# Kernel tuning notes

Hardware: AMD Instinct MI355X
Metric: run time of the kernel (lower is better)

## Reference

```python
import jax, jax.numpy as jnp
import numpy as np

GRID_DIM = 7  # margin = 0, so each grid cell is a disjoint (H//g, W//g) tile


def setup_inputs() -> dict:
    key = jax.random.key(0)
    k1, k2 = jax.random.split(key)
    B, H, W, C = 8, 224, 224, 256
    NQ = 64
    images = jax.random.normal(k1, (B, H, W, C), dtype=jnp.float32)
    queries = jax.random.normal(k2, (NQ, C), dtype=jnp.float32)
    return {"images": images, "queries": queries}


def reference(images, queries):
    # images: [B, H, W, C]; queries: [NQ, C]
    B, H, W, C = images.shape
    g = GRID_DIM
    hs, ws = H // g, W // g  # tile size per grid cell (margin = 0)
    # Crop all g*g cells at once: [B, g, hs, g, ws, C] -> [B, g*g, L, C]
    # Cell index n = i*g + j (i over height, j over width) matches the
    # original positions ordering (pos[0] -> height, pos[1] -> width).
    regions = images.reshape(B, g, hs, g, ws, C)
    regions = regions.transpose(0, 1, 3, 2, 4, 5).reshape(B, g * g, hs * ws, C)
    # keras.layers.Attention default: unscaled dot-product + softmax.
    scores = jnp.einsum('qc,bnlc->bnql', queries, regions)  # [B, g*g, NQ, L]
    attn = jax.nn.softmax(scores, axis=-1)
    out = jnp.einsum('bnql,bnlc->bnqc', attn, regions)      # [B, g*g, NQ, C]
    return out
```

## Files before the change

kernel.cpp:

```cpp
#include <hip/hip_runtime.h>

typedef _Float16 half8 __attribute__((ext_vector_type(8)));
typedef _Float16 half4 __attribute__((ext_vector_type(4)));
typedef __fp16   fp16x2 __attribute__((ext_vector_type(2)));
typedef float f32x4  __attribute__((ext_vector_type(4)));

#define DEVI __device__ __forceinline__

constexpr int Bc = 8;
constexpr int Hc = 224;
constexpr int Wc = 224;
constexpr int Cc = 256;
constexpr int NQ = 64;
constexpr int TS = 32;
constexpr int Lc = TS * TS;
constexpr int KL = 64;
constexpr int NT = Lc / KL;

constexpr long PSTRIDE = 64 * 256 * 2 + 64 * 4 + 64 * 4;
constexpr long WS_NEED = 784 * PSTRIDE;

DEVI int subidx(int l, int c) {
  return ((((l >> 2) << 4) | (c >> 4)) << 6) | (((l & 3) << 4) | (c & 15));
}

DEVI uint ldsoff(const void* p) {
  return (uint)(uintptr_t)(const __attribute__((address_space(3))) char*)p;
}

union PKU { fp16x2 h; uint u; };
DEVI uint pkrtz(float a, float b) { PKU x; x.h = __builtin_amdgcn_cvt_pkrtz(a, b); return x.u; }
union HBU { _Float16 h; ushort u; };
DEVI ushort hbits(float x) { HBU v; v.h = (_Float16)x; return v.u; }

__global__ __launch_bounds__(256, 2) void attn_cells(
    const float* __restrict__ img,
    const float* __restrict__ qry,
    float* __restrict__ out,
    char* __restrict__ wsp,
    int splt)
{
  __shared__ _Float16 Rlds[2][KL * Cc];
  __shared__ _Float16 Plds[4][16 * KL];
  __shared__ float    Slds[NQ];
  __shared__ float    Llds[NQ];

  const int tid  = threadIdx.x;
  const int w    = tid >> 6;
  const int lane = tid & 63;
  const int lp   = lane & 15;
  const int gq   = lane >> 4;

  const int bx = blockIdx.x;
  const int bn = splt ? (bx >> 1) : bx;
  const int h  = splt ? (bx & 1)  : 0;
  const int tbeg = h * 8;
  const int tend = tbeg + (splt ? 8 : NT);

  const int b  = bn / 49;
  const int n  = bn % 49;
  const int i0 = n / 7, j0 = n % 7;

  const long cellbase = (((long)b * Hc + i0 * TS) * Wc + j0 * TS) * Cc;

  int goff[8], lds_off[8];
  #pragma unroll
  for (int s = 0; s < 8; ++s) {
    int G   = s * 256 + tid;
    int blk = G >> 3, sub = G & 7;
    int l   = ((blk >> 4) << 2) | ((sub >> 1) & 3);
    int c   = ((blk & 15) << 4) | ((sub & 1) << 3);
    int y   = l >> 5, x = l & 31;
    goff[s]    = (y * Wc + x) * Cc + c;
    lds_off[s] = G << 3;
  }

  half8 bq[8];
  {
    const int qrow = (w << 4) | lp;
    #pragma unroll
    for (int kc = 0; kc < 8; ++kc) {
      const float* qp = &qry[qrow * Cc + kc * 32 + gq * 8];
      f32x4 lo = *(const f32x4*)qp;
      f32x4 hi = *(const f32x4*)(qp + 4);
      half8 hh;
      #pragma unroll
      for (int j = 0; j < 4; ++j) { hh[j] = (_Float16)lo[j]; hh[j + 4] = (_Float16)hi[j]; }
      bq[kc] = hh;
    }
  }

  f32x4 acc[4][4];
  #pragma unroll
  for (int qb = 0; qb < 4; ++qb)
    #pragma unroll
    for (int cb = 0; cb < 4; ++cb) acc[qb][cb] = f32x4{0.f, 0.f, 0.f, 0.f};

  float mrun = -3.0e38f;
  float lsum = 0.0f;

  {
    const float* gb = img + cellbase + (long)tbeg * (2 * Wc * Cc);
    #pragma unroll
    for (int s = 0; s < 8; ++s) {
      f32x4 lo = *(const f32x4*)&gb[goff[s]];
      f32x4 hi = *(const f32x4*)&gb[goff[s] + 4];
      uint4 pk;
      pk.x = pkrtz(lo[0], lo[1]); pk.y = pkrtz(lo[2], lo[3]);
      pk.z = pkrtz(hi[0], hi[1]); pk.w = pkrtz(hi[2], hi[3]);
      *(uint4*)&Rlds[0][lds_off[s]] = pk;
    }
  }
  __syncthreads();

  const uint trlane = (uint)(gq * 4096 + w * 512 +
                             ((((lp >> 2) << 4) | ((lp & 3) << 2)) << 1));

  for (int t = tbeg; t < tend; ++t) {
    const int pb = t & 1;
    const _Float16* Rbuf = &Rlds[pb][0];
    const uint trbase = ldsoff(Rbuf) + trlane;

    if (t + 1 < tend) {
      const float* gb = img + cellbase + (long)(t + 1) * (2 * Wc * Cc);
      _Float16* Rn = &Rlds[pb ^ 1][0];
      #pragma unroll
      for (int s = 0; s < 8; ++s) {
        f32x4 lo = *(const f32x4*)&gb[goff[s]];
        f32x4 hi = *(const f32x4*)&gb[goff[s] + 4];
        uint4 pk;
        pk.x = pkrtz(lo[0], lo[1]); pk.y = pkrtz(lo[2], lo[3]);
        pk.z = pkrtz(hi[0], hi[1]); pk.w = pkrtz(hi[2], hi[3]);
        *(uint4*)&Rn[lds_off[s]] = pk;
      }
    }

    f32x4 sv[4];
    #pragma unroll
    for (int lb = 0; lb < 4; ++lb) sv[lb] = f32x4{0.f, 0.f, 0.f, 0.f};
    #pragma unroll
    for (int kc = 0; kc < 8; ++kc) {
      #pragma unroll
      for (int lb = 0; lb < 4; ++lb) {
        half8 a = *(const half8*)&Rbuf[subidx(lb * 16 + lp, kc * 32 + gq * 8)];
        sv[lb] = __builtin_amdgcn_mfma_f32_16x16x32_f16(a, bq[kc], sv[lb], 0, 0, 0);
      }
    }

    float cmax = sv[0][0];
    #pragma unroll
    for (int lb = 0; lb < 4; ++lb)
      #pragma unroll
      for (int r = 0; r < 4; ++r) cmax = fmaxf(cmax, sv[lb][r]);
    cmax = fmaxf(cmax, __shfl_xor(cmax, 16));
    cmax = fmaxf(cmax, __shfl_xor(cmax, 32));

    float mnew  = fmaxf(mrun, cmax);
    float scale = __expf(mrun - mnew);

    float ps = 0.0f;
    float pv[4][4];
    #pragma unroll
    for (int lb = 0; lb < 4; ++lb)
      #pragma unroll
      for (int r = 0; r < 4; ++r) {
        float p = __expf(sv[lb][r] - mnew);
        pv[lb][r] = p; ps += p;
      }
    ps += __shfl_xor(ps, 16);
    ps += __shfl_xor(ps, 32);
    lsum = lsum * scale + ps;
    mrun = mnew;

    {
      char* Pw = (char*)&Plds[w][0];
      #pragma unroll
      for (int lb = 0; lb < 4; ++lb) {
        uint lo = pkrtz(pv[lb][0], pv[lb][1]);
        uint hi = pkrtz(pv[lb][2], pv[lb][3]);
        int base = lp * 128 + lb * 32 + gq * 8;
        int swz  = (lp & 7) << 4;
        *(uint*)(Pw + ((base ^ swz)))     = lo;
        *(uint*)(Pw + ((base ^ swz) + 4)) = hi;
      }
      if (lane < 16) Slds[w * 16 + lp] = scale;
    }

    __syncthreads();

    #pragma unroll
    for (int qb = 0; qb < 4; ++qb) {
      f32x4 sc = *(const f32x4*)&Slds[qb * 16 + gq * 4];
      #pragma unroll
      for (int cb = 0; cb < 4; ++cb) acc[qb][cb] *= sc;
    }

    #pragma unroll
    for (int kc = 0; kc < 2; ++kc) {
      half8 pa[4];
      #pragma unroll
      for (int qb = 0; qb < 4; ++qb) {
        const char* Pr = (const char*)&Plds[qb][0];
        int off = (lp * 128 + gq * 16 + kc * 64) ^ ((lp & 7) << 4);
        pa[qb] = *(const half8*)(Pr + off);
      }
      half4 tr[4][2];
      #pragma unroll
      for (int cb = 0; cb < 4; ++cb) {
        #pragma unroll
        for (int u = 0; u < 2; ++u) {
          asm volatile("ds_read_b64_tr_b16 %0, %1 offset:%2"
                       : "=v"(tr[cb][u])
                       : "v"(trbase), "i"(kc * 16384 + u * 2048 + cb * 128));
        }
      }
      asm volatile("s_waitcnt lgkmcnt(0)" ::: "memory");
      __builtin_amdgcn_sched_barrier(0);

      #pragma unroll
      for (int qb = 0; qb < 4; ++qb)
        #pragma unroll
        for (int cb = 0; cb < 4; ++cb) {
          half8 bv = __builtin_shufflevector(tr[cb][0], tr[cb][1], 0, 1, 2, 3, 4, 5, 6, 7);
          acc[qb][cb] = __builtin_amdgcn_mfma_f32_16x16x32_f16(pa[qb], bv, acc[qb][cb], 0, 0, 0);
        }
    }

    __syncthreads();
  }

  if (splt) {
    char* pbase = wsp + (long)bx * PSTRIDE;
    #pragma unroll
    for (int qb = 0; qb < 4; ++qb)
      #pragma unroll
      for (int r = 0; r < 4; ++r) {
        const int q = qb * 16 + gq * 4 + r;
        #pragma unroll
        for (int cb = 0; cb < 4; ++cb) {
          const int c = w * 64 + cb * 16 + lp;
          *(ushort*)(pbase + (q * 256 + c) * 2) = hbits(acc[qb][cb][r]);
        }
      }
    if (lane < 16) {
      const int q = w * 16 + lp;
      *(float*)(pbase + 32768 + q * 4) = mrun;
      *(float*)(pbase + 33024 + q * 4) = lsum;
    }
  } else {
    if (lane < 16) Llds[w * 16 + lp] = lsum;
    __syncthreads();
    float* ob = out + (long)bn * NQ * Cc;
    #pragma unroll
    for (int qb = 0; qb < 4; ++qb) {
      f32x4 lv = *(const f32x4*)&Llds[qb * 16 + gq * 4];
      #pragma unroll
      for (int r = 0; r < 4; ++r) {
        const float iv = 1.0f / lv[r];
        const int q = qb * 16 + gq * 4 + r;
        #pragma unroll
        for (int cb = 0; cb < 4; ++cb) {
          const int c = w * 64 + cb * 16 + lp;
          ob[q * Cc + c] = acc[qb][cb][r] * iv;
        }
      }
    }
  }
}

__global__ __launch_bounds__(256) void combine_halves(
    const char* __restrict__ ws, float* __restrict__ out)
{
  const int cell = blockIdx.x >> 1;
  const int qh   = blockIdx.x & 1;
  const int t    = threadIdx.x;

  const char* p0 = ws + (long)(cell * 2 + 0) * PSTRIDE;
  const char* p1 = ws + (long)(cell * 2 + 1) * PSTRIDE;
  float* ob = out + (long)cell * (NQ * Cc);

  #pragma unroll
  for (int v = 0; v < 4; ++v) {
    const int f = qh * 8192 + v * 2048 + t * 8;
    const int q = f >> 8;
    const float m0 = *(const float*)(p0 + 32768 + q * 4);
    const float m1 = *(const float*)(p1 + 32768 + q * 4);
    const float l0 = *(const float*)(p0 + 33024 + q * 4);
    const float l1 = *(const float*)(p1 + 33024 + q * 4);
    const float M  = fmaxf(m0, m1);
    const float a0 = __expf(m0 - M), a1 = __expf(m1 - M);
    const float inv = 1.0f / (a0 * l0 + a1 * l1);

    half8 x0 = *(const half8*)(p0 + (long)f * 2);
    half8 x1 = *(const half8*)(p1 + (long)f * 2);
    float* o = ob + f;
    #pragma unroll
    for (int j = 0; j < 8; ++j)
      o[j] = (a0 * (float)x0[j] + a1 * (float)x1[j]) * inv;
  }
}

extern "C" void kernel_launch(void* const* d_in, const int* in_sizes, int n_in,
                              void* d_out, int out_size, void* d_ws, size_t ws_size,
                              hipStream_t stream) {
  const float* img = (const float*)d_in[0];
  const float* qry = (const float*)d_in[1];
  float* outp      = (float*)d_out;
  if (ws_size >= (size_t)WS_NEED) {
    attn_cells<<<dim3(Bc * 49 * 2), dim3(256), 0, stream>>>(img, qry, outp, (char*)d_ws, 1);
    combine_halves<<<dim3(Bc * 49 * 2), dim3(256), 0, stream>>>((const char*)d_ws, outp);
  } else {
    attn_cells<<<dim3(Bc * 49), dim3(256), 0, stream>>>(img, qry, outp, (char*)d_ws, 0);
  }
}
```

Measured before the change: 114.1 us.

## Halve key tile to 32 rows to raise occupancy to three blocks per CU

Shrinks the per-iteration key tile from 64 to 32 positions (one image row of the cell), halving the double-buffered LDS region and score registers, and raises launch bounds to 3 blocks per CU. The PV stage now does a single 32-wide k-chunk per step, and the exp/pack code is interleaved to cut live registers. The intent is more concurrent blocks to hide global-load latency, at the cost of twice as many iterations with barriers and rescale work per tile.

```diff
diff --git a/kernel.cpp b/kernel.cpp
--- a/kernel.cpp
+++ b/kernel.cpp
@@ -14,7 +14,7 @@
 constexpr int NQ = 64;
 constexpr int TS = 32;
 constexpr int Lc = TS * TS;
-constexpr int KL = 64;
+constexpr int KL = 32;
 constexpr int NT = Lc / KL;
 
 constexpr long PSTRIDE = 64 * 256 * 2 + 64 * 4 + 64 * 4;
@@ -33,7 +33,7 @@
 union HBU { _Float16 h; ushort u; };
 DEVI ushort hbits(float x) { HBU v; v.h = (_Float16)x; return v.u; }
 
-__global__ __launch_bounds__(256, 2) void attn_cells(
+__global__ __launch_bounds__(256, 3) void attn_cells(
     const float* __restrict__ img,
     const float* __restrict__ qry,
     float* __restrict__ out,
@@ -41,7 +41,7 @@
     int splt)
 {
   __shared__ _Float16 Rlds[2][KL * Cc];
-  __shared__ _Float16 Plds[4][16 * KL];
+  __shared__ _Float16 Plds[4][16 * 64];
   __shared__ float    Slds[NQ];
   __shared__ float    Llds[NQ];
 
@@ -54,8 +54,8 @@
   const int bx = blockIdx.x;
   const int bn = splt ? (bx >> 1) : bx;
   const int h  = splt ? (bx & 1)  : 0;
-  const int tbeg = h * 8;
-  const int tend = tbeg + (splt ? 8 : NT);
+  const int tbeg = h * 16;
+  const int tend = tbeg + (splt ? 16 : NT);
 
   const int b  = bn / 49;
   const int n  = bn % 49;
@@ -63,15 +63,14 @@
 
   const long cellbase = (((long)b * Hc + i0 * TS) * Wc + j0 * TS) * Cc;
 
-  int goff[8], lds_off[8];
+  int goff[4], lds_off[4];
   #pragma unroll
-  for (int s = 0; s < 8; ++s) {
+  for (int s = 0; s < 4; ++s) {
     int G   = s * 256 + tid;
     int blk = G >> 3, sub = G & 7;
     int l   = ((blk >> 4) << 2) | ((sub >> 1) & 3);
     int c   = ((blk & 15) << 4) | ((sub & 1) << 3);
-    int y   = l >> 5, x = l & 31;
-    goff[s]    = (y * Wc + x) * Cc + c;
+    goff[s]    = l * Cc + c;
     lds_off[s] = G << 3;
   }
 
@@ -100,9 +99,9 @@
   float lsum = 0.0f;
 
   {
-    const float* gb = img + cellbase + (long)tbeg * (2 * Wc * Cc);
-    #pragma unroll
-    for (int s = 0; s < 8; ++s) {
+    const float* gb = img + cellbase + (long)tbeg * (Wc * Cc);
+    #pragma unroll
+    for (int s = 0; s < 4; ++s) {
       f32x4 lo = *(const f32x4*)&gb[goff[s]];
       f32x4 hi = *(const f32x4*)&gb[goff[s] + 4];
       uint4 pk;
@@ -122,10 +121,10 @@
     const uint trbase = ldsoff(Rbuf) + trlane;
 
     if (t + 1 < tend) {
-      const float* gb = img + cellbase + (long)(t + 1) * (2 * Wc * Cc);
+      const float* gb = img + cellbase + (long)(t + 1) * (Wc * Cc);
       _Float16* Rn = &Rlds[pb ^ 1][0];
       #pragma unroll
-      for (int s = 0; s < 8; ++s) {
+      for (int s = 0; s < 4; ++s) {
         f32x4 lo = *(const f32x4*)&gb[goff[s]];
         f32x4 hi = *(const f32x4*)&gb[goff[s] + 4];
         uint4 pk;
@@ -135,13 +134,13 @@
       }
     }
 
-    f32x4 sv[4];
-    #pragma unroll
-    for (int lb = 0; lb < 4; ++lb) sv[lb] = f32x4{0.f, 0.f, 0.f, 0.f};
+    f32x4 sv[2];
+    #pragma unroll
+    for (int lb = 0; lb < 2; ++lb) sv[lb] = f32x4{0.f, 0.f, 0.f, 0.f};
     #pragma unroll
     for (int kc = 0; kc < 8; ++kc) {
       #pragma unroll
-      for (int lb = 0; lb < 4; ++lb) {
+      for (int lb = 0; lb < 2; ++lb) {
         half8 a = *(const half8*)&Rbuf[subidx(lb * 16 + lp, kc * 32 + gq * 8)];
         sv[lb] = __builtin_amdgcn_mfma_f32_16x16x32_f16(a, bq[kc], sv[lb], 0, 0, 0);
       }
@@ -149,7 +148,7 @@
 
     float cmax = sv[0][0];
     #pragma unroll
-    for (int lb = 0; lb < 4; ++lb)
+    for (int lb = 0; lb < 2; ++lb)
       #pragma unroll
       for (int r = 0; r < 4; ++r) cmax = fmaxf(cmax, sv[lb][r]);
     cmax = fmaxf(cmax, __shfl_xor(cmax, 16));
@@ -159,33 +158,27 @@
     float scale = __expf(mrun - mnew);
 
     float ps = 0.0f;
-    float pv[4][4];
-    #pragma unroll
-    for (int lb = 0; lb < 4; ++lb)
-      #pragma unroll
-      for (int r = 0; r < 4; ++r) {
-        float p = __expf(sv[lb][r] - mnew);
-        pv[lb][r] = p; ps += p;
-      }
+    {
+      char* Pw = (char*)&Plds[w][0];
+      #pragma unroll
+      for (int lb = 0; lb < 2; ++lb) {
+        float p0 = __expf(sv[lb][0] - mnew);
+        float p1 = __expf(sv[lb][1] - mnew);
+        float p2 = __expf(sv[lb][2] - mnew);
+        float p3 = __expf(sv[lb][3] - mnew);
+        ps += (p0 + p1) + (p2 + p3);
+        int base = lp * 128 + lb * 32 + gq * 8;
+        int swz  = (lp & 7) << 4;
+        *(uint*)(Pw + ((base ^ swz)))     = pkrtz(p0, p1);
+        *(uint*)(Pw + ((base ^ swz) + 4)) = pkrtz(p2, p3);
+      }
+      if (lane < 16) Slds[w * 16 + lp] = scale;
+    }
     ps += __shfl_xor(ps, 16);
     ps += __shfl_xor(ps, 32);
     lsum = lsum * scale + ps;
     mrun = mnew;
 
-    {
-      char* Pw = (char*)&Plds[w][0];
-      #pragma unroll
-      for (int lb = 0; lb < 4; ++lb) {
-        uint lo = pkrtz(pv[lb][0], pv[lb][1]);
-        uint hi = pkrtz(pv[lb][2], pv[lb][3]);
-        int base = lp * 128 + lb * 32 + gq * 8;
-        int swz  = (lp & 7) << 4;
-        *(uint*)(Pw + ((base ^ swz)))     = lo;
-        *(uint*)(Pw + ((base ^ swz) + 4)) = hi;
-      }
-      if (lane < 16) Slds[w * 16 + lp] = scale;
-    }
-
     __syncthreads();
 
     #pragma unroll
@@ -195,13 +188,12 @@
       for (int cb = 0; cb < 4; ++cb) acc[qb][cb] *= sc;
     }
 
-    #pragma unroll
-    for (int kc = 0; kc < 2; ++kc) {
+    {
       half8 pa[4];
       #pragma unroll
       for (int qb = 0; qb < 4; ++qb) {
         const char* Pr = (const char*)&Plds[qb][0];
-        int off = (lp * 128 + gq * 16 + kc * 64) ^ ((lp & 7) << 4);
+        int off = (lp * 128 + gq * 16) ^ ((lp & 7) << 4);
         pa[qb] = *(const half8*)(Pr + off);
       }
       half4 tr[4][2];
@@ -211,7 +203,7 @@
         for (int u = 0; u < 2; ++u) {
           asm volatile("ds_read_b64_tr_b16 %0, %1 offset:%2"
                        : "=v"(tr[cb][u])
-                       : "v"(trbase), "i"(kc * 16384 + u * 2048 + cb * 128));
+                       : "v"(trbase), "i"(u * 2048 + cb * 128));
         }
       }
       asm volatile("s_waitcnt lgkmcnt(0)" ::: "memory");
```

After: 149.0 us. 1.31x slower.

## Split only a subset of cells into halves, run the rest as full blocks

Applied to the files above, without the earlier changes.

Changes the work decomposition so the first 256 cells are processed by single full-length blocks that write final output directly, while only the remaining 136 cells are split across two half-blocks and merged by the combine kernel. This cuts workspace writes and combine-kernel launches and aims to balance the grid against the CU count. It risks load imbalance, since full blocks take twice as long as half blocks and the grid may not pack evenly into resident slots.

```diff
diff --git a/kernel.cpp b/kernel.cpp
--- a/kernel.cpp
+++ b/kernel.cpp
@@ -17,8 +17,12 @@
 constexpr int KL = 64;
 constexpr int NT = Lc / KL;
 
+constexpr int NFULL  = 256;
+constexpr int NSPLIT = 392 - NFULL;
+constexpr int NHALF  = NSPLIT * 2;
+
 constexpr long PSTRIDE = 64 * 256 * 2 + 64 * 4 + 64 * 4;
-constexpr long WS_NEED = 784 * PSTRIDE;
+constexpr long WS_NEED = (long)NHALF * PSTRIDE;
 
 DEVI int subidx(int l, int c) {
   return ((((l >> 2) << 4) | (c >> 4)) << 6) | (((l & 3) << 4) | (c & 15));
@@ -52,10 +56,19 @@
   const int gq   = lane >> 4;
 
   const int bx = blockIdx.x;
-  const int bn = splt ? (bx >> 1) : bx;
-  const int h  = splt ? (bx & 1)  : 0;
-  const int tbeg = h * 8;
-  const int tend = tbeg + (splt ? 8 : NT);
+  int bn, tbeg, tend, pslot;
+  if (splt && bx >= NFULL) {
+    const int s = bx - NFULL;
+    bn    = NFULL + (s >> 1);
+    tbeg  = (s & 1) * (NT / 2);
+    tend  = tbeg + NT / 2;
+    pslot = s;
+  } else {
+    bn    = bx;
+    tbeg  = 0;
+    tend  = NT;
+    pslot = -1;
+  }
 
   const int b  = bn / 49;
   const int n  = bn % 49;
@@ -229,8 +242,8 @@
     __syncthreads();
   }
 
-  if (splt) {
-    char* pbase = wsp + (long)bx * PSTRIDE;
+  if (pslot >= 0) {
+    char* pbase = wsp + (long)pslot * PSTRIDE;
     #pragma unroll
     for (int qb = 0; qb < 4; ++qb)
       #pragma unroll
@@ -271,12 +284,14 @@
 __global__ __launch_bounds__(256) void combine_halves(
     const char* __restrict__ ws, float* __restrict__ out)
 {
-  const int cell = blockIdx.x >> 1;
-  const int qh   = blockIdx.x & 1;
+  const int s    = blockIdx.x;
+  const int ci   = s >> 1;
+  const int cell = NFULL + ci;
+  const int qh   = s & 1;
   const int t    = threadIdx.x;
 
-  const char* p0 = ws + (long)(cell * 2 + 0) * PSTRIDE;
-  const char* p1 = ws + (long)(cell * 2 + 1) * PSTRIDE;
+  const char* p0 = ws + (long)(ci * 2 + 0) * PSTRIDE;
+  const char* p1 = ws + (long)(ci * 2 + 1) * PSTRIDE;
   float* ob = out + (long)cell * (NQ * Cc);
 
   #pragma unroll
@@ -307,8 +322,8 @@
   const float* qry = (const float*)d_in[1];
   float* outp      = (float*)d_out;
   if (ws_size >= (size_t)WS_NEED) {
-    attn_cells<<<dim3(Bc * 49 * 2), dim3(256), 0, stream>>>(img, qry, outp, (char*)d_ws, 1);
-    combine_halves<<<dim3(Bc * 49 * 2), dim3(256), 0, stream>>>((const char*)d_ws, outp);
+    attn_cells<<<dim3(NFULL + NHALF), dim3(256), 0, stream>>>(img, qry, outp, (char*)d_ws, 1);
+    combine_halves<<<dim3(NHALF), dim3(256), 0, stream>>>((const char*)d_ws, outp);
   } else {
     attn_cells<<<dim3(Bc * 49), dim3(256), 0, stream>>>(img, qry, outp, (char*)d_ws, 0);
   }
```

New measurement: 107.6 us. -5.7%, faster.
